# Optimization experiments

Measured on AMD Instinct MI355X. Metric: run time of the kernel, lower is better.

## Reference

```python
import jax, jax.numpy as jnp
import numpy as np

BINS = 10
MOMENTUM = 0.75  # first-call acc_sum = (1 - MOMENTUM) * num_in_bin (acc_sum starts at 0)
BS, CLA = 1048576, 32


def _smooth(bins):
    s = 1.0 - 25.0 * (np.arange(bins, dtype=np.float64) / bins) ** 2
    s[int(bins * 0.2):] = 0.0
    s[s < 0] = 0.0
    return jnp.asarray(s, jnp.float32)


def setup_inputs() -> dict:
    key = jax.random.key(0)
    k1, k2, k3 = jax.random.split(key, 3)
    targets = jax.random.bernoulli(k1, 0.5, (BS, CLA)).astype(jnp.float32)
    # per-row noise scale so g = mean|inputs-targets| spreads over the low bins (<0.3)
    row_scale = jax.random.uniform(k3, (BS, 1), minval=0.01, maxval=0.3)
    noise = jax.random.uniform(k2, (BS, CLA)) * row_scale
    inputs = jnp.clip(jnp.abs(targets - noise), 1e-4, 1.0 - 1e-4)
    return {"inputs": inputs, "targets": targets}


def reference(inputs, targets):
    bins, m = BINS, MOMENTUM
    bs, cla = inputs.shape
    tot = float(bs * cla)
    # g uses inputs.detach(); binning/weighting is non-differentiable anyway
    g = jax.lax.stop_gradient(jnp.mean(jnp.abs(inputs - targets), axis=1))  # [bs]
    # edges are i/bins (last edge 1+1e-6): bin index = floor(g*bins), clipped
    idx = jnp.clip(jnp.floor(g * bins).astype(jnp.int32), 0, bins - 1)
    counts = jnp.zeros((bins,), jnp.float32).at[idx].add(1.0)  # histogram
    acc_sum = (1.0 - m) * counts  # momentum update from acc_sum=0
    smooth = _smooth(bins)
    safe_acc = jnp.where(acc_sum > 0, acc_sum, 1.0)
    per_bin_w = jnp.where(counts > 0, smooth * tot / safe_acc, 0.0)  # [bins]
    w = per_bin_w[idx]  # [bs]
    w = w * w
    w = w / jnp.sum(w)
    w = jnp.where(w < 1e-6, 0.0, w)
    # elementwise BCE on probabilities, mean over classes, weighted sum over batch
    loss_el = -(targets * jnp.log(inputs) + (1.0 - targets) * jnp.log1p(-inputs))
    return jnp.sum(jnp.mean(loss_el, axis=1) * w)
```

## Files before the change

kernel.cpp:

```cpp
#include <hip/hip_runtime.h>

#define BS_ROWS 1048576
#define CLA 32
#define NBINS 10
#define GRID 2048
#define RPB 512
#define BATCH 8
#define OUTER 2

template <int CTRL>
__device__ __forceinline__ float dpp_add(float v) {
    int x = __builtin_amdgcn_update_dpp(0, __float_as_int(v), CTRL, 0xF, 0xF, true);
    return v + __int_as_float(x);
}
#define DPP_XOR1 0xB1
#define DPP_XOR2 0x4E
#define DPP_HMIR 0x141

__global__ __launch_bounds__(256, 4) void ghm_pass1(
    const float* __restrict__ in, const float* __restrict__ tg,
    float* __restrict__ cnt, float* __restrict__ bsum)
{
    __shared__ float s_cnt[NBINS];
    __shared__ float s_bsum[NBINS];
    const int tid = threadIdx.x;
    if (tid < NBINS) { s_cnt[tid] = 0.0f; s_bsum[tid] = 0.0f; }
    __syncthreads();

    const unsigned sub = tid & 7;
    const unsigned rg  = tid >> 3;
    const float4* __restrict__ in4 = (const float4*)in;
    const float4* __restrict__ tg4 = (const float4*)tg;
    const unsigned base = blockIdx.x * (RPB * CLA / 4);

    #pragma unroll 1
    for (int outer = 0; outer < OUTER; ++outer) {
        float4 iv[BATCH], tv[BATCH];
        #pragma unroll
        for (int j = 0; j < BATCH; ++j) {
            const unsigned fi = base + (unsigned)(outer * BATCH + j) * 256u
                              + rg * 8u + sub;
            iv[j] = in4[fi];
            tv[j] = tg4[fi];
        }

        float garr[BATCH], barr[BATCH];
        #pragma unroll
        for (int j = 0; j < BATCH; ++j) {
            float gp = fabsf(iv[j].x - tv[j].x) + fabsf(iv[j].y - tv[j].y)
                     + fabsf(iv[j].z - tv[j].z) + fabsf(iv[j].w - tv[j].w);
            float a0 = tv[j].x > 0.5f ? iv[j].x : 1.0f - iv[j].x;
            float a1 = tv[j].y > 0.5f ? iv[j].y : 1.0f - iv[j].y;
            float a2 = tv[j].z > 0.5f ? iv[j].z : 1.0f - iv[j].z;
            float a3 = tv[j].w > 0.5f ? iv[j].w : 1.0f - iv[j].w;
            float bp = -(__logf(a0) + __logf(a1) + __logf(a2) + __logf(a3));

            gp = dpp_add<DPP_XOR1>(gp);  bp = dpp_add<DPP_XOR1>(bp);
            gp = dpp_add<DPP_XOR2>(gp);  bp = dpp_add<DPP_XOR2>(bp);
            gp = dpp_add<DPP_HMIR>(gp);  bp = dpp_add<DPP_HMIR>(bp);
            garr[j] = gp;  barr[j] = bp;
        }

        if (sub == 0) {
            #pragma unroll
            for (int j = 0; j < BATCH; ++j) {
                float g = garr[j] * (1.0f / 32.0f);
                int bi = (int)(g * 10.0f);
                bi = bi < 0 ? 0 : (bi > NBINS - 1 ? NBINS - 1 : bi);
                atomicAdd(&s_cnt[bi], 1.0f);
                atomicAdd(&s_bsum[bi], barr[j] * (1.0f / 32.0f));
            }
        }
    }

    __syncthreads();
    if (tid < NBINS) {
        atomicAdd(&cnt[tid], s_cnt[tid]);
        atomicAdd(&bsum[tid], s_bsum[tid]);
    }
}

__global__ void ghm_pass2(const float* __restrict__ cnt,
                          const float* __restrict__ bsum,
                          float* __restrict__ out)
{
    if (threadIdx.x == 0 && blockIdx.x == 0) {
        const double tot = (double)BS_ROWS * (double)CLA;
        const float smooth[NBINS] = {1.0f, 0.75f, 0,0,0,0,0,0,0,0};
        double pbw2[NBINS];
        double sum_w = 0.0;
        for (int b = 0; b < NBINS; ++b) {
            double c = (double)cnt[b];
            double pbw = (c > 0.0 && smooth[b] > 0.0f)
                       ? (double)smooth[b] * tot / (0.25 * c) : 0.0;
            pbw2[b] = pbw * pbw;
            sum_w += c * pbw2[b];
        }
        double loss = 0.0;
        for (int b = 0; b < NBINS; ++b) {
            double w = (sum_w > 0.0) ? pbw2[b] / sum_w : 0.0;
            if (w < 1e-6) w = 0.0;
            loss += (double)bsum[b] * w;
        }
        out[0] = (float)loss;
    }
}

extern "C" void kernel_launch(void* const* d_in, const int* in_sizes, int n_in,
                              void* d_out, int out_size, void* d_ws, size_t ws_size,
                              hipStream_t stream) {
    const float* in = (const float*)d_in[0];
    const float* tg = (const float*)d_in[1];
    float* ws   = (float*)d_ws;
    float* cnt  = ws;
    float* bsum = ws + NBINS;

    (void)hipMemsetAsync(d_ws, 0, 2 * NBINS * sizeof(float), stream);

    ghm_pass1<<<GRID, 256, 0, stream>>>(in, tg, cnt, bsum);
    ghm_pass2<<<1, 64, 0, stream>>>(cnt, bsum, (float*)d_out);
}
```

Baseline: 80.71 us.

## Accumulate only nonzero-weight bins in registers instead of LDS atomics

Replaces the per-row shared-memory atomic histogram with per-thread register accumulators that track only bins 0 and 1, the only bins with nonzero smoothing weight. These are reduced with wave shuffles and a few LDS and global atomics. It also changes batching from 8x2 to 4x4 and raises the occupancy hint in launch bounds. The aim is to remove serialized LDS atomics and divergent sub==0 work from a bandwidth-bound kernel. The trade-off is that counts for higher bins are no longer produced, and the shared reduction buffer is initialized without a barrier before the atomics.

```diff
diff --git a/kernel.cpp b/kernel.cpp
--- a/kernel.cpp
+++ b/kernel.cpp
@@ -5,8 +5,8 @@
 #define NBINS 10
 #define GRID 2048
 #define RPB 512
-#define BATCH 8
-#define OUTER 2
+#define BATCH 4
+#define OUTER 4
 
 template <int CTRL>
 __device__ __forceinline__ float dpp_add(float v) {
@@ -17,34 +17,32 @@
 #define DPP_XOR2 0x4E
 #define DPP_HMIR 0x141
 
-__global__ __launch_bounds__(256, 4) void ghm_pass1(
+__global__ __launch_bounds__(256, 8) void ghm_pass1(
     const float* __restrict__ in, const float* __restrict__ tg,
     float* __restrict__ cnt, float* __restrict__ bsum)
 {
-    __shared__ float s_cnt[NBINS];
-    __shared__ float s_bsum[NBINS];
+    __shared__ float red[4];
     const int tid = threadIdx.x;
-    if (tid < NBINS) { s_cnt[tid] = 0.0f; s_bsum[tid] = 0.0f; }
-    __syncthreads();
+    if (tid < 4) red[tid] = 0.0f;
 
     const unsigned sub = tid & 7;
-    const unsigned rg  = tid >> 3;
     const float4* __restrict__ in4 = (const float4*)in;
     const float4* __restrict__ tg4 = (const float4*)tg;
-    const unsigned base = blockIdx.x * (RPB * CLA / 4);
+    const unsigned base = blockIdx.x * (RPB * CLA / 4) + (unsigned)tid;
+
+    float c0 = 0.0f, c1 = 0.0f, b0 = 0.0f, b1 = 0.0f;
 
     #pragma unroll 1
     for (int outer = 0; outer < OUTER; ++outer) {
         float4 iv[BATCH], tv[BATCH];
         #pragma unroll
         for (int j = 0; j < BATCH; ++j) {
-            const unsigned fi = base + (unsigned)(outer * BATCH + j) * 256u
-                              + rg * 8u + sub;
+            const unsigned fi = base + (unsigned)(outer * BATCH + j) * 256u;
             iv[j] = in4[fi];
             tv[j] = tg4[fi];
         }
+        asm volatile("" ::: "memory");
 
-        float garr[BATCH], barr[BATCH];
         #pragma unroll
         for (int j = 0; j < BATCH; ++j) {
             float gp = fabsf(iv[j].x - tv[j].x) + fabsf(iv[j].y - tv[j].y)
@@ -58,25 +56,40 @@
             gp = dpp_add<DPP_XOR1>(gp);  bp = dpp_add<DPP_XOR1>(bp);
             gp = dpp_add<DPP_XOR2>(gp);  bp = dpp_add<DPP_XOR2>(bp);
             gp = dpp_add<DPP_HMIR>(gp);  bp = dpp_add<DPP_HMIR>(bp);
-            garr[j] = gp;  barr[j] = bp;
-        }
 
-        if (sub == 0) {
-            #pragma unroll
-            for (int j = 0; j < BATCH; ++j) {
-                float g = garr[j] * (1.0f / 32.0f);
-                int bi = (int)(g * 10.0f);
-                bi = bi < 0 ? 0 : (bi > NBINS - 1 ? NBINS - 1 : bi);
-                atomicAdd(&s_cnt[bi], 1.0f);
-                atomicAdd(&s_bsum[bi], barr[j] * (1.0f / 32.0f));
-            }
+            float g = gp * (1.0f / 32.0f);
+            int bi = (int)(g * 10.0f);
+            bool v0 = (sub == 0) && (bi == 0);
+            bool v1 = (sub == 0) && (bi == 1);
+            c0 += v0 ? 1.0f : 0.0f;
+            c1 += v1 ? 1.0f : 0.0f;
+            b0 += v0 ? bp : 0.0f;
+            b1 += v1 ? bp : 0.0f;
         }
     }
 
+    b0 *= (1.0f / 32.0f);
+    b1 *= (1.0f / 32.0f);
+
+    #pragma unroll
+    for (int off = 8; off < 64; off <<= 1) {
+        c0 += __shfl_xor(c0, off);
+        c1 += __shfl_xor(c1, off);
+        b0 += __shfl_xor(b0, off);
+        b1 += __shfl_xor(b1, off);
+    }
+    if ((tid & 63) == 0) {
+        atomicAdd(&red[0], c0);
+        atomicAdd(&red[1], c1);
+        atomicAdd(&red[2], b0);
+        atomicAdd(&red[3], b1);
+    }
     __syncthreads();
-    if (tid < NBINS) {
-        atomicAdd(&cnt[tid], s_cnt[tid]);
-        atomicAdd(&bsum[tid], s_bsum[tid]);
+    if (tid == 0) {
+        atomicAdd(&cnt[0],  red[0]);
+        atomicAdd(&cnt[1],  red[1]);
+        atomicAdd(&bsum[0], red[2]);
+        atomicAdd(&bsum[1], red[3]);
     }
 }
 
```

Result: slower. 131.1 us (+62.4%).
